# Optimization experiments

Measured on AMD Instinct MI355X. Metric: run time of the kernel, lower is better.

The kernel has to match this reference:

```python
import jax, jax.numpy as jnp
import numpy as np

N_NODES = 10000   # n_entity
VOCAB = 50000     # nvoc
EMBED = 300       # nembed
HID = 256         # nhid
REP = 8           # words per node name


def setup_inputs() -> dict:
    key = jax.random.key(0)
    k0, k1, k2, k3, k4 = jax.random.split(key, 5)
    nodes_rep = jax.random.randint(k0, (N_NODES + 1, REP), 0, VOCAB)
    emb = jax.random.normal(k1, (VOCAB, EMBED), dtype=jnp.float32) * 0.02
    # dense (row-scaled) adjacency, as the module does adj @ support
    adj = jax.random.uniform(k2, (N_NODES, N_NODES), dtype=jnp.float32) / N_NODES
    W1 = jax.random.normal(k3, (EMBED, HID), dtype=jnp.float32) * 0.05
    b1 = jnp.zeros((HID,), dtype=jnp.float32)
    W2 = jax.random.normal(k4, (HID, HID), dtype=jnp.float32) * 0.05
    b2 = jnp.zeros((HID,), dtype=jnp.float32)
    return {"nodes_rep": nodes_rep, "emb": emb, "adj": adj,
            "W1": W1, "b1": b1, "W2": W2, "b2": b2}


def reference(nodes_rep, emb, adj, W1, b1, W2, b2):
    # get_nodes_embed, model == 'gcn_no_dropout'
    x = emb[nodes_rep[1:]]            # [N, REP, EMBED] gather
    x = jnp.max(x, axis=1)            # max-pool over name words -> [N, EMBED]
    # GraphConvolution: adj @ (x @ W) + b
    h = jax.nn.leaky_relu(adj @ (x @ W1) + b1)   # [N, HID]
    h = jax.nn.leaky_relu(adj @ (h @ W2) + b2)   # [N, HID]
    return h
```

## Files before the change

kernel.cpp:

```cpp
#include <hip/hip_runtime.h>
#include <stdint.h>


#define N_NODES 10000
#define MP      10112
#define KP      10048
#define EMB     300
#define EKP     320
#define HID     256
#define SLOPE   0.01f
#define NSPLIT  8
#define KCHUNK  1280

typedef __attribute__((ext_vector_type(8))) short          bf16x8;
typedef __attribute__((ext_vector_type(4))) float          f32x4;
typedef __attribute__((ext_vector_type(8))) unsigned short ushort8;
typedef __attribute__((ext_vector_type(4))) unsigned short ushort4v;

__device__ __forceinline__ unsigned short f2b(float f) {
    union { float f; unsigned u; } v; v.f = f;
    unsigned r = v.u + 0x7FFFu + ((v.u >> 16) & 1u);
    return (unsigned short)(r >> 16);
}

__device__ __forceinline__ void g2l16(const void* gptr, const void* ldsptr) {
    __builtin_amdgcn_global_load_lds(
        (const __attribute__((address_space(1))) void*)(uintptr_t)gptr,
        (__attribute__((address_space(3))) void*)(uint32_t)(uintptr_t)ldsptr,
        16, 0, 0);
}

__global__ void convert_adj(const float* __restrict__ adj,
                            unsigned short* __restrict__ out) {
    const int r  = blockIdx.y;
    const int c0 = (blockIdx.x * 256 + threadIdx.x) * 8;
    if (c0 >= KP) return;
    ushort8 v = {};
    if (r < N_NODES && c0 + 8 <= N_NODES) {
        const float* src = adj + (size_t)r * N_NODES + c0;
        f32x4 f0 = *(const f32x4*)src;
        f32x4 f1 = *(const f32x4*)(src + 4);
#pragma unroll
        for (int t = 0; t < 4; ++t) { v[t] = f2b(f0[t]); v[t + 4] = f2b(f1[t]); }
    }
    *(ushort8*)(out + (size_t)r * KP + c0) = v;
}

__global__ void gather_max_x(const int* __restrict__ nodes,
                             const float* __restrict__ emb,
                             unsigned short* __restrict__ xb) {
    const int i = blockIdx.x;
    unsigned short* xrow = xb + (size_t)i * EKP;
    if (i >= N_NODES) {
        for (int e = threadIdx.x; e < EKP; e += 256) xrow[e] = 0;
        return;
    }
    const int* idx = nodes + (i + 1) * 8;
    int id[8];
#pragma unroll
    for (int r = 0; r < 8; ++r) id[r] = idx[r];
    for (int e = threadIdx.x; e < EKP; e += 256) {
        unsigned short v = 0;
        if (e < EMB) {
            float m = emb[(size_t)id[0] * EMB + e];
#pragma unroll
            for (int r = 1; r < 8; ++r) m = fmaxf(m, emb[(size_t)id[r] * EMB + e]);
            v = f2b(m);
        }
        xrow[e] = v;
    }
}

__global__ void prep_w(const float* __restrict__ W, unsigned short* __restrict__ Wt,
                       int K, int Kpad) {
    const int o = blockIdx.x * 256 + threadIdx.x;
    if (o >= HID * Kpad) return;
    const int n = o / Kpad, k = o % Kpad;
    Wt[o] = (k < K) ? f2b(W[(size_t)k * HID + n]) : 0;
}

__global__ void transpose_bf16(const unsigned short* __restrict__ in,
                               unsigned short* __restrict__ out) {
    __shared__ unsigned short t[32][33];
    const int kt = blockIdx.x * 32, nt = blockIdx.y * 32;
    const int x = threadIdx.x, y0 = threadIdx.y;
#pragma unroll
    for (int yy = y0; yy < 32; yy += 8)
        t[yy][x] = in[(size_t)(kt + yy) * HID + nt + x];
    __syncthreads();
#pragma unroll
    for (int yy = y0; yy < 32; yy += 8)
        out[(size_t)(nt + yy) * KP + kt + x] = t[x][yy];
}

template <int MODE>
__global__ void gemm_bt(const unsigned short* __restrict__ A, int ldA,
                        const unsigned short* __restrict__ Bt, int ldB,
                        void* __restrict__ Cout, int ldC,
                        int Ktot, int kChunk, size_t partStride) {
    const int tid  = threadIdx.x;
    const int wave = tid >> 6, lane = tid & 63;
    const int wm = wave >> 1, wn = wave & 1;
    const int l16 = lane & 15, quad = lane >> 4;
    const int tileM = blockIdx.x * 128;
    const int tileN = blockIdx.y * 128;
    const int kStart = (MODE == 1) ? (int)blockIdx.z * kChunk : 0;
    const int kLen   = min(kChunk, Ktot - kStart);

    __shared__ unsigned short ldsA[128 * 64];
    __shared__ unsigned short ldsB[128 * 64];

    const unsigned short* Ag = A  + (size_t)(tileM + (tid >> 3)) * ldA + kStart + ((tid & 7) * 8);
    const unsigned short* Bg = Bt + (size_t)(tileN + (tid >> 3)) * ldB + kStart + ((tid & 7) * 8);
    unsigned short* lA = &ldsA[tid * 8];
    unsigned short* lB = &ldsB[tid * 8];
    const size_t aStep = (size_t)32 * ldA;
    const size_t bStep = (size_t)32 * ldB;

    const unsigned short* pa0 = &ldsA[(wm * 64 + l16) * 64 + quad * 8];
    const unsigned short* pb0 = &ldsB[(wn * 64 + l16) * 64 + quad * 8];

    f32x4 acc[4][4] = {};
    const int kIters = kLen >> 6;

    for (int kt = 0; kt < kIters; ++kt) {
        __syncthreads();
#pragma unroll
        for (int i = 0; i < 4; ++i) {
            g2l16(Ag + i * aStep, lA + i * 2048);
            g2l16(Bg + i * bStep, lB + i * 2048);
        }
        Ag += 64; Bg += 64;
        __syncthreads();
#pragma unroll
        for (int kk = 0; kk < 64; kk += 32) {
            bf16x8 af[4], bq[4];
#pragma unroll
            for (int i = 0; i < 4; ++i) af[i] = *(const bf16x8*)(pa0 + i * 1024 + kk);
#pragma unroll
            for (int j = 0; j < 4; ++j) bq[j] = *(const bf16x8*)(pb0 + j * 1024 + kk);
#pragma unroll
            for (int i = 0; i < 4; ++i)
#pragma unroll
                for (int j = 0; j < 4; ++j)
                    acc[i][j] = __builtin_amdgcn_mfma_f32_16x16x32_bf16(
                        af[i], bq[j], acc[i][j], 0, 0, 0);
        }
    }

    if (MODE == 0) {
        unsigned short* C = (unsigned short*)Cout;
#pragma unroll
        for (int i = 0; i < 4; ++i)
#pragma unroll
            for (int r = 0; r < 4; ++r) {
                const int row = tileM + wm * 64 + i * 16 + quad * 4 + r;
#pragma unroll
                for (int j = 0; j < 4; ++j) {
                    const int col = tileN + wn * 64 + j * 16 + l16;
                    C[(size_t)row * ldC + col] = f2b(acc[i][j][r]);
                }
            }
    } else {
        float* C = (float*)Cout + (size_t)blockIdx.z * partStride;
#pragma unroll
        for (int i = 0; i < 4; ++i)
#pragma unroll
            for (int r = 0; r < 4; ++r) {
                const int row = tileM + wm * 64 + i * 16 + quad * 4 + r;
#pragma unroll
                for (int j = 0; j < 4; ++j) {
                    const int col = tileN + wn * 64 + j * 16 + l16;
                    C[(size_t)row * ldC + col] = acc[i][j][r];
                }
            }
    }
}

template <int OUT_BF16, int NPART>
__global__ void reduce_bias_lrelu(const float* __restrict__ parts, size_t partStride,
                                  const float* __restrict__ bias,
                                  void* __restrict__ out, int outRows) {
    const int idx = blockIdx.x * 256 + threadIdx.x;
    const int e4  = idx * 4;
    const int row = e4 >> 8;
    const int col = e4 & 255;
    if (row >= MP) return;
    f32x4 s = *(const f32x4*)(parts + e4);
#pragma unroll
    for (int p = 1; p < NPART; ++p) s += *(const f32x4*)(parts + p * partStride + e4);
    s += *(const f32x4*)(bias + col);
#pragma unroll
    for (int t = 0; t < 4; ++t) s[t] = s[t] > 0.0f ? s[t] : SLOPE * s[t];
    if (OUT_BF16) {
        ushort4v o;
#pragma unroll
        for (int t = 0; t < 4; ++t) o[t] = f2b(s[t]);
        *(ushort4v*)((unsigned short*)out + e4) = o;
    } else if (row < outRows) {
        *(f32x4*)((float*)out + e4) = s;
    }
}

extern "C" void kernel_launch(void* const* d_in, const int* in_sizes, int n_in,
                              void* d_out, int out_size, void* d_ws, size_t ws_size,
                              hipStream_t stream) {
    const int*   nodes = (const int*)d_in[0];
    const float* emb   = (const float*)d_in[1];
    const float* adj   = (const float*)d_in[2];
    const float* W1    = (const float*)d_in[3];
    const float* b1    = (const float*)d_in[4];
    const float* W2    = (const float*)d_in[5];
    const float* b2    = (const float*)d_in[6];

    char* ws = (char*)d_ws;
    size_t o = 0;
    unsigned short* adjb = (unsigned short*)(ws + o); o += (size_t)MP * KP * 2;
    unsigned short* xb   = (unsigned short*)(ws + o); o += (size_t)MP * EKP * 2;
    unsigned short* w1t  = (unsigned short*)(ws + o); o += (size_t)HID * EKP * 2;
    unsigned short* w2t  = (unsigned short*)(ws + o); o += (size_t)HID * HID * 2;
    unsigned short* u1   = (unsigned short*)(ws + o); o += (size_t)MP * HID * 2;
    unsigned short* u1t  = (unsigned short*)(ws + o); o += (size_t)HID * KP * 2;
    unsigned short* h1   = (unsigned short*)(ws + o); o += (size_t)MP * HID * 2;
    unsigned short* u2   = (unsigned short*)(ws + o); o += (size_t)MP * HID * 2;
    unsigned short* u2t  = (unsigned short*)(ws + o); o += (size_t)HID * KP * 2;
    float*          parts= (float*)(ws + o);          o += (size_t)NSPLIT * MP * HID * 4;

    const size_t PSTRIDE = (size_t)MP * HID;

    convert_adj <<<dim3(5, MP), 256, 0, stream>>>(adj, adjb);
    gather_max_x<<<MP, 256, 0, stream>>>(nodes, emb, xb);
    prep_w      <<<(HID * EKP + 255) / 256, 256, 0, stream>>>(W1, w1t, EMB, EKP);
    prep_w      <<<(HID * HID + 255) / 256, 256, 0, stream>>>(W2, w2t, HID, HID);

    gemm_bt<0><<<dim3(79, 2, 1), 256, 0, stream>>>(xb, EKP, w1t, EKP, u1, HID,
                                                   EKP, EKP, 0);
    transpose_bf16<<<dim3(KP / 32, HID / 32), dim3(32, 8), 0, stream>>>(u1, u1t);

    gemm_bt<1><<<dim3(79, 2, NSPLIT), 256, 0, stream>>>(adjb, KP, u1t, KP, parts, HID,
                                                        KP, KCHUNK, PSTRIDE);
    reduce_bias_lrelu<1, NSPLIT><<<(MP * HID / 4 + 255) / 256, 256, 0, stream>>>(
        parts, PSTRIDE, b1, h1, MP);

    gemm_bt<0><<<dim3(79, 2, 1), 256, 0, stream>>>(h1, HID, w2t, HID, u2, HID,
                                                   HID, HID, 0);
    transpose_bf16<<<dim3(KP / 32, HID / 32), dim3(32, 8), 0, stream>>>(u2, u2t);

    gemm_bt<1><<<dim3(79, 2, NSPLIT), 256, 0, stream>>>(adjb, KP, u2t, KP, parts, HID,
                                                        KP, KCHUNK, PSTRIDE);
    reduce_bias_lrelu<0, NSPLIT><<<(MP * HID / 4 + 255) / 256, 256, 0, stream>>>(
        parts, PSTRIDE, b2, d_out, N_NODES);
}
```

Before: 841.4 us.

## Widen GEMM tile to full hidden width and emit transposed projections directly

The GEMM kernel now uses 512 threads (8 waves) and a 128x256 tile, so each adjacency GEMM block covers all 256 hidden columns. Each adjacency row block is therefore streamed once per layer instead of once for each of two N-tiles. The small projection GEMMs swap their operands so they write the transposed U matrix directly, which removes both transpose kernels and their extra memory round-trips. MP is padded to 10240 to fit the 256-wide tiles. The cost is more LDS per block and fewer blocks, which may lower occupancy.

```diff
diff --git a/kernel.cpp b/kernel.cpp
--- a/kernel.cpp
+++ b/kernel.cpp
@@ -3,7 +3,7 @@
 
 
 #define N_NODES 10000
-#define MP      10112
+#define MP      10240
 #define KP      10048
 #define EMB     300
 #define EKP     320
@@ -79,20 +79,6 @@
     Wt[o] = (k < K) ? f2b(W[(size_t)k * HID + n]) : 0;
 }
 
-__global__ void transpose_bf16(const unsigned short* __restrict__ in,
-                               unsigned short* __restrict__ out) {
-    __shared__ unsigned short t[32][33];
-    const int kt = blockIdx.x * 32, nt = blockIdx.y * 32;
-    const int x = threadIdx.x, y0 = threadIdx.y;
-#pragma unroll
-    for (int yy = y0; yy < 32; yy += 8)
-        t[yy][x] = in[(size_t)(kt + yy) * HID + nt + x];
-    __syncthreads();
-#pragma unroll
-    for (int yy = y0; yy < 32; yy += 8)
-        out[(size_t)(nt + yy) * KP + kt + x] = t[x][yy];
-}
-
 template <int MODE>
 __global__ void gemm_bt(const unsigned short* __restrict__ A, int ldA,
                         const unsigned short* __restrict__ Bt, int ldB,
@@ -100,22 +86,22 @@
                         int Ktot, int kChunk, size_t partStride) {
     const int tid  = threadIdx.x;
     const int wave = tid >> 6, lane = tid & 63;
-    const int wm = wave >> 1, wn = wave & 1;
+    const int wm = wave >> 2, wn = wave & 3;
     const int l16 = lane & 15, quad = lane >> 4;
     const int tileM = blockIdx.x * 128;
-    const int tileN = blockIdx.y * 128;
+    const int tileN = blockIdx.y * 256;
     const int kStart = (MODE == 1) ? (int)blockIdx.z * kChunk : 0;
     const int kLen   = min(kChunk, Ktot - kStart);
 
     __shared__ unsigned short ldsA[128 * 64];
-    __shared__ unsigned short ldsB[128 * 64];
+    __shared__ unsigned short ldsB[256 * 64];
 
     const unsigned short* Ag = A  + (size_t)(tileM + (tid >> 3)) * ldA + kStart + ((tid & 7) * 8);
     const unsigned short* Bg = Bt + (size_t)(tileN + (tid >> 3)) * ldB + kStart + ((tid & 7) * 8);
     unsigned short* lA = &ldsA[tid * 8];
     unsigned short* lB = &ldsB[tid * 8];
-    const size_t aStep = (size_t)32 * ldA;
-    const size_t bStep = (size_t)32 * ldB;
+    const size_t aStep = (size_t)64 * ldA;
+    const size_t bStep = (size_t)64 * ldB;
 
     const unsigned short* pa0 = &ldsA[(wm * 64 + l16) * 64 + quad * 8];
     const unsigned short* pb0 = &ldsB[(wn * 64 + l16) * 64 + quad * 8];
@@ -126,10 +112,9 @@
     for (int kt = 0; kt < kIters; ++kt) {
         __syncthreads();
 #pragma unroll
-        for (int i = 0; i < 4; ++i) {
-            g2l16(Ag + i * aStep, lA + i * 2048);
-            g2l16(Bg + i * bStep, lB + i * 2048);
-        }
+        for (int i = 0; i < 2; ++i) g2l16(Ag + i * aStep, lA + i * 4096);
+#pragma unroll
+        for (int i = 0; i < 4; ++i) g2l16(Bg + i * bStep, lB + i * 4096);
         Ag += 64; Bg += 64;
         __syncthreads();
 #pragma unroll
@@ -219,11 +204,9 @@
     unsigned short* xb   = (unsigned short*)(ws + o); o += (size_t)MP * EKP * 2;
     unsigned short* w1t  = (unsigned short*)(ws + o); o += (size_t)HID * EKP * 2;
     unsigned short* w2t  = (unsigned short*)(ws + o); o += (size_t)HID * HID * 2;
-    unsigned short* u1   = (unsigned short*)(ws + o); o += (size_t)MP * HID * 2;
-    unsigned short* u1t  = (unsigned short*)(ws + o); o += (size_t)HID * KP * 2;
+    unsigned short* u1t  = (unsigned short*)(ws + o); o += (size_t)HID * MP * 2;
     unsigned short* h1   = (unsigned short*)(ws + o); o += (size_t)MP * HID * 2;
-    unsigned short* u2   = (unsigned short*)(ws + o); o += (size_t)MP * HID * 2;
-    unsigned short* u2t  = (unsigned short*)(ws + o); o += (size_t)HID * KP * 2;
+    unsigned short* u2t  = (unsigned short*)(ws + o); o += (size_t)HID * MP * 2;
     float*          parts= (float*)(ws + o);          o += (size_t)NSPLIT * MP * HID * 4;
 
     const size_t PSTRIDE = (size_t)MP * HID;
@@ -233,21 +216,19 @@
     prep_w      <<<(HID * EKP + 255) / 256, 256, 0, stream>>>(W1, w1t, EMB, EKP);
     prep_w      <<<(HID * HID + 255) / 256, 256, 0, stream>>>(W2, w2t, HID, HID);
 
-    gemm_bt<0><<<dim3(79, 2, 1), 256, 0, stream>>>(xb, EKP, w1t, EKP, u1, HID,
-                                                   EKP, EKP, 0);
-    transpose_bf16<<<dim3(KP / 32, HID / 32), dim3(32, 8), 0, stream>>>(u1, u1t);
-
-    gemm_bt<1><<<dim3(79, 2, NSPLIT), 256, 0, stream>>>(adjb, KP, u1t, KP, parts, HID,
-                                                        KP, KCHUNK, PSTRIDE);
+    gemm_bt<0><<<dim3(2, MP / 256, 1), 512, 0, stream>>>(w1t, EKP, xb, EKP,
+                                                         u1t, MP, EKP, EKP, 0);
+
+    gemm_bt<1><<<dim3(MP / 128, 1, NSPLIT), 512, 0, stream>>>(adjb, KP, u1t, MP,
+                                                              parts, HID, KP, KCHUNK, PSTRIDE);
     reduce_bias_lrelu<1, NSPLIT><<<(MP * HID / 4 + 255) / 256, 256, 0, stream>>>(
         parts, PSTRIDE, b1, h1, MP);
 
-    gemm_bt<0><<<dim3(79, 2, 1), 256, 0, stream>>>(h1, HID, w2t, HID, u2, HID,
-                                                   HID, HID, 0);
-    transpose_bf16<<<dim3(KP / 32, HID / 32), dim3(32, 8), 0, stream>>>(u2, u2t);
-
-    gemm_bt<1><<<dim3(79, 2, NSPLIT), 256, 0, stream>>>(adjb, KP, u2t, KP, parts, HID,
-                                                        KP, KCHUNK, PSTRIDE);
+    gemm_bt<0><<<dim3(2, MP / 256, 1), 512, 0, stream>>>(w2t, HID, h1, HID,
+                                                         u2t, MP, HID, HID, 0);
+
+    gemm_bt<1><<<dim3(MP / 128, 1, NSPLIT), 512, 0, stream>>>(adjb, KP, u2t, MP,
+                                                              parts, HID, KP, KCHUNK, PSTRIDE);
     reduce_bias_lrelu<0, NSPLIT><<<(MP * HID / 4 + 255) / 256, 256, 0, stream>>>(
         parts, PSTRIDE, b2, d_out, N_NODES);
 }
```

Measured after the change: 859.4 us. 1.02x slower.
